# Kernel tuning notes

Measured on AMD Instinct MI355X. Metric: run time of the kernel, lower is better.

## Reference

```python
import jax, jax.numpy as jnp
import numpy as np

CLASS_COUNT = 21
THRESHOLD = 0.5
ALPHA = 0.25
GAMMA = 2.0
VARIANCE = (0.1, 0.2)

B, A, N_OBJ = 32, 24576, 16


def point_form(boxes):
    # center form (cx, cy, w, h) -> point form (xmin, ymin, xmax, ymax)
    return jnp.concatenate([boxes[:, :2] - boxes[:, 2:] / 2,
                            boxes[:, :2] + boxes[:, 2:] / 2], axis=1)


def jaccard(truths, priors):
    # truths [N,4], priors [A,4] both in point form -> IoU [N, A]
    lt = jnp.maximum(truths[:, None, :2], priors[None, :, :2])
    rb = jnp.minimum(truths[:, None, 2:], priors[None, :, 2:])
    wh = jnp.clip(rb - lt, 0.0, None)
    inter = wh[..., 0] * wh[..., 1]
    area_t = ((truths[:, 2] - truths[:, 0]) * (truths[:, 3] - truths[:, 1]))[:, None]
    area_p = ((priors[:, 2] - priors[:, 0]) * (priors[:, 3] - priors[:, 1]))[None, :]
    return inter / (area_t + area_p - inter)


def match_one(labels, truths, anchors):
    # labels [N] int, truths [N,4] point form, anchors [A,4] center form
    overlaps = jaccard(truths, point_form(anchors))           # [N, A]
    best_prior_idx = jnp.argmax(overlaps, axis=1)             # [N]
    best_truth_overlap = jnp.max(overlaps, axis=0)            # [A]
    best_truth_idx = jnp.argmax(overlaps, axis=0)             # [A]
    # ensure every gt matches its best prior
    best_truth_overlap = best_truth_overlap.at[best_prior_idx].set(2.0)
    best_truth_idx = best_truth_idx.at[best_prior_idx].set(jnp.arange(truths.shape[0]))
    matches = truths[best_truth_idx]                          # [A, 4]
    conf = jnp.where(best_truth_overlap < THRESHOLD, 0, labels[best_truth_idx])
    # encode with variances
    g_cxcy = ((matches[:, :2] + matches[:, 2:]) * 0.5 - anchors[:, :2]) / (VARIANCE[0] * anchors[:, 2:])
    g_wh = jnp.log((matches[:, 2:] - matches[:, :2]) / anchors[:, 2:]) / VARIANCE[1]
    return conf, jnp.concatenate([g_cxcy, g_wh], axis=1)


def setup_inputs() -> dict:
    key = jax.random.key(0)
    k1, k2, k3, k4, k5, k6, k7 = jax.random.split(key, 7)
    class_preds = jax.random.normal(k1, (B, A, CLASS_COUNT), dtype=jnp.float32)
    loc_preds = jax.random.normal(k2, (B, A, 4), dtype=jnp.float32)
    # ground-truth boxes: random valid point-form boxes in [0,1]
    ctr = jax.random.uniform(k3, (B, N_OBJ, 2), minval=0.2, maxval=0.8)
    wh = jax.random.uniform(k4, (B, N_OBJ, 2), minval=0.05, maxval=0.3)
    loc_targets = jnp.clip(jnp.concatenate([ctr - wh / 2, ctr + wh / 2], axis=-1), 0.0, 1.0)
    class_targets = jax.random.randint(k5, (B, N_OBJ), 1, CLASS_COUNT)
    # anchors in center form
    a_ctr = jax.random.uniform(k6, (A, 2), minval=0.05, maxval=0.95)
    a_wh = jax.random.uniform(k7, (A, 2), minval=0.05, maxval=0.4)
    anchors = jnp.concatenate([a_ctr, a_wh], axis=1)
    return {"class_preds": class_preds, "loc_preds": loc_preds,
            "loc_targets": loc_targets, "anchors": anchors,
            "class_targets": class_targets}


def reference(class_preds, loc_preds, loc_targets, anchors, class_targets):
    conf, loc_t = jax.vmap(match_one, in_axes=(0, 0, None))(class_targets, loc_targets, anchors)
    pos = conf > 0                                            # [B, A]
    num_matched = jnp.sum(pos).astype(jnp.float32)
    # smooth L1 over positive anchors (sum reduction, beta=1)
    d = loc_preds - loc_t
    ad = jnp.abs(d)
    sl1 = jnp.where(ad < 1.0, 0.5 * d * d, ad - 0.5)
    loc_loss = jnp.sum(sl1 * pos[..., None].astype(sl1.dtype))
    # focal loss (drop background column 0)
    cp = class_preds.reshape(-1, CLASS_COUNT)[:, 1:]          # [B*A, C-1]
    t = jax.nn.one_hot(conf.reshape(-1), CLASS_COUNT, dtype=cp.dtype)[:, 1:]
    p = jax.nn.sigmoid(cp)
    pt = jnp.where(t > 0, p, 1.0 - p)
    w = (1.0 - pt) ** GAMMA
    w = jnp.where(t > 0, ALPHA * w, (1.0 - ALPHA) * w)
    # stable binary cross entropy with logits, weighted, sum reduction
    bce = jnp.maximum(cp, 0.0) - cp * t + jnp.log1p(jnp.exp(-jnp.abs(cp)))
    class_loss = jnp.sum(w * bce)
    class_loss = class_loss / num_matched
    loc_loss = loc_loss / num_matched
    return jnp.stack([class_loss, loc_loss, class_loss + loc_loss])
```

## Files before the change

kernel.cpp:

```cpp
#include <hip/hip_runtime.h>

#define A_COUNT 24576
#define B_COUNT 32
#define NOBJ 16
#define C_COUNT 21

#define NCH 96
#define CHUNK (A_COUNT / NCH)
#define NBLK (NCH * B_COUNT)
#define TOTAL4 (B_COUNT * A_COUNT * C_COUNT / 4)
#define STRIDE4 (NBLK * 256)

#define WS_BPP 0
#define WS_LOCP 393216
#define WS_CLSP 405504
#define WS_POSP 417792
#define WS_DLOC 430080
#define WS_DCLS 430208
#define WS_DPOS 430336

__device__ __forceinline__ unsigned long long pack_key(float iou, int a) {
    unsigned int ib = __float_as_uint(iou);
    return ((unsigned long long)ib << 32) | (unsigned long long)(0xFFFFFFFFu - (unsigned int)a);
}

__device__ __forceinline__ float iou_pf(float tx0, float ty0, float tx1, float ty1, float at,
                                        float x0, float y0, float x1, float y1, float ap) {
    float lx = fmaxf(tx0, x0), ly = fmaxf(ty0, y0);
    float rx = fminf(tx1, x1), ry = fminf(ty1, y1);
    float w = fmaxf(rx - lx, 0.0f), h = fmaxf(ry - ly, 0.0f);
    float inter = w * h;
    return inter * __builtin_amdgcn_rcpf(at + ap - inter);
}

__device__ __forceinline__ float sl1(float d) {
    float ad = fabsf(d);
    return (ad < 1.0f) ? 0.5f * d * d : ad - 0.5f;
}

__device__ __forceinline__ float loc_term(float4 t, float4 an, float4 lp) {
    float gx = ((t.x + t.z) * 0.5f - an.x) / (0.1f * an.z);
    float gy = ((t.y + t.w) * 0.5f - an.y) / (0.1f * an.w);
    float gw = __logf((t.z - t.x) / an.z) * 5.0f;
    float gh = __logf((t.w - t.y) / an.w) * 5.0f;
    return sl1(lp.x - gx) + sl1(lp.y - gy) + sl1(lp.z - gw) + sl1(lp.w - gh);
}

__device__ __forceinline__ float corr_term(float x) {
    float E = __expf(x);
    float den = 1.0f + E;
    float s = __builtin_amdgcn_rcpf(den);
    float p = E * s;
    float L = __logf(den);
    return 0.25f * s * s * (L - x) - 0.75f * p * p * L;
}

#define FOC(xval, rr, acc) {                                 \
    float E_ = __expf(xval);                                 \
    float den_ = 1.0f + E_;                                  \
    float s_ = __builtin_amdgcn_rcpf(den_);                  \
    float p_ = E_ * s_;                                      \
    float L_ = __logf(den_);                                 \
    float v_ = ((rr) == 0 || (rr) == 21) ? 0.0f : p_ * p_ * L_; \
    acc += v_; }

__global__ __launch_bounds__(256, 8) void k_main(const float* __restrict__ cls,
                                                 const float4* __restrict__ locp,
                                                 const float4* __restrict__ anchors,
                                                 const float4* __restrict__ truths,
                                                 const int* __restrict__ labels,
                                                 unsigned long long* __restrict__ bp_partial,
                                                 float* __restrict__ loc_partial,
                                                 float* __restrict__ cls_partial,
                                                 unsigned int* __restrict__ pos_partial) {
    const int ch = blockIdx.x;
    const int b = blockIdx.y;
    const int tid = threadIdx.x;
    const int wv = tid >> 6, ln = tid & 63;
    __shared__ float4 s_t[NOBJ];
    __shared__ float s_area[NOBJ];
    __shared__ int s_lab[NOBJ];
    __shared__ unsigned long long s_w[NOBJ][4];
    if (tid < NOBJ) {
        float4 t = truths[b * NOBJ + tid];
        s_t[tid] = t;
        s_area[tid] = (t.z - t.x) * (t.w - t.y);
        s_lab[tid] = labels[b * NOBJ + tid];
    }
    __syncthreads();
    const int a0 = ch * CHUNK + tid;
    float4 an0 = anchors[a0];
    float p0x0 = an0.x - an0.z * 0.5f, p0y0 = an0.y - an0.w * 0.5f;
    float p0x1 = an0.x + an0.z * 0.5f, p0y1 = an0.y + an0.w * 0.5f;
    float ap0 = (p0x1 - p0x0) * (p0y1 - p0y0);
    float best0 = -1.0f;
    int idx0 = 0;
#pragma unroll
    for (int n = 0; n < NOBJ; ++n) {
        float4 t = s_t[n];
        float iou = iou_pf(t.x, t.y, t.z, t.w, s_area[n], p0x0, p0y0, p0x1, p0y1, ap0);
        if (iou > best0) { best0 = iou; idx0 = n; }
        float m = iou;
#pragma unroll
        for (int s = 32; s >= 1; s >>= 1) m = fmaxf(m, __shfl_xor(m, s));
        unsigned long long mask = __ballot(iou == m);
        if (ln == __builtin_ctzll(mask))
            s_w[n][wv] = pack_key(iou, a0);
    }
    __syncthreads();
    if (tid < NOBJ) {
        unsigned long long k = s_w[tid][0];
#pragma unroll
        for (int i = 1; i < 4; ++i) k = (s_w[tid][i] > k) ? s_w[tid][i] : k;
        bp_partial[(b * NOBJ + tid) * NCH + ch] = k;
    }
    float loc_l = 0.0f, corr_acc = 0.0f;
    unsigned int pos = 0;
    if (!(best0 < 0.5f)) {
        pos = 1;
        loc_l = loc_term(s_t[idx0], an0, locp[(size_t)b * A_COUNT + a0]);
        corr_acc = corr_term(cls[((size_t)b * A_COUNT + a0) * C_COUNT + s_lab[idx0]]);
    }

    const int bid = b * NCH + ch;
    float cls_acc;
    {
        const float4* cls4 = (const float4*)cls;
        int i = bid * 256 + tid;
        unsigned int f = (unsigned int)i * 4u;
        unsigned int dq = f / 21u;
        int r = (int)(f - dq * 21u);
        float acc0 = 0.0f, acc1 = 0.0f, acc2 = 0.0f, acc3 = 0.0f;
        for (; i < TOTAL4; i += STRIDE4) {
            float4 x4 = cls4[i];
            FOC(x4.x, r + 0, acc0); FOC(x4.y, r + 1, acc1);
            FOC(x4.z, r + 2, acc2); FOC(x4.w, r + 3, acc3);
            r += 12; if (r >= 21) r -= 21;
        }
        cls_acc = corr_acc + 0.75f * ((acc0 + acc1) + (acc2 + acc3));
    }

#pragma unroll
    for (int s = 32; s >= 1; s >>= 1) {
        loc_l += __shfl_xor(loc_l, s);
        cls_acc += __shfl_xor(cls_acc, s);
        pos += __shfl_xor(pos, s);
    }
    __shared__ float s_ll[4], s_cl[4];
    __shared__ unsigned int s_pp[4];
    if (ln == 0) {
        s_ll[wv] = loc_l;
        s_cl[wv] = cls_acc;
        s_pp[wv] = pos;
    }
    __syncthreads();
    if (tid == 0) {
        loc_partial[bid] = s_ll[0] + s_ll[1] + s_ll[2] + s_ll[3];
        cls_partial[bid] = s_cl[0] + s_cl[1] + s_cl[2] + s_cl[3];
        pos_partial[bid] = s_pp[0] + s_pp[1] + s_pp[2] + s_pp[3];
    }
}

__global__ __launch_bounds__(256) void k_fix(const float* __restrict__ cls,
                                             const float4* __restrict__ locp,
                                             const float4* __restrict__ anchors,
                                             const float4* __restrict__ truths,
                                             const int* __restrict__ labels,
                                             const unsigned long long* __restrict__ bp_partial,
                                             float* __restrict__ dloc,
                                             float* __restrict__ dcls,
                                             int* __restrict__ dpos) {
    const int b = blockIdx.x;
    const int tid = threadIdx.x;
    __shared__ int s_bp[NOBJ];
    {
        const int g = tid >> 4, l = tid & 15;
        const unsigned long long* pp = &bp_partial[(size_t)(b * NOBJ + g) * NCH];
        unsigned long long k = pp[l];
#pragma unroll
        for (int kk = 1; kk < 6; ++kk) {
            unsigned long long v = pp[l + 16 * kk];
            k = (v > k) ? v : k;
        }
#pragma unroll
        for (int s = 8; s >= 1; s >>= 1) {
            unsigned long long o = __shfl_xor(k, s);
            k = (o > k) ? o : k;
        }
        if (l == 0) {
            unsigned int ia = 0xFFFFFFFFu - (unsigned int)(k & 0xFFFFFFFFull);
            s_bp[g] = (ia >= A_COUNT) ? -1 : (int)ia;
        }
    }
    __syncthreads();
    float d_loc = 0.0f, d_cls = 0.0f;
    int d_pos = 0;
    if (tid < NOBJ) {
        const int n = tid;
        const int q = s_bp[n];
        bool winner = (q >= 0);
        for (int n2 = n + 1; n2 < NOBJ; ++n2)
            if (s_bp[n2] == q) winner = false;
        if (winner) {
            float4 an = anchors[q];
            float px0 = an.x - an.z * 0.5f, py0 = an.y - an.w * 0.5f;
            float px1 = an.x + an.z * 0.5f, py1 = an.y + an.w * 0.5f;
            float ap = (px1 - px0) * (py1 - py0);
            float best = -1.0f;
            int idx = 0;
            for (int n2 = 0; n2 < NOBJ; ++n2) {
                float4 t = truths[b * NOBJ + n2];
                float at = (t.z - t.x) * (t.w - t.y);
                float iou = iou_pf(t.x, t.y, t.z, t.w, at, px0, py0, px1, py1, ap);
                if (iou > best) { best = iou; idx = n2; }
            }
            float4 lp = locp[(size_t)b * A_COUNT + q];
            if (!(best < 0.5f)) {
                d_pos -= 1;
                d_loc -= loc_term(truths[b * NOBJ + idx], an, lp);
                d_cls -= corr_term(cls[((size_t)b * A_COUNT + q) * C_COUNT + labels[b * NOBJ + idx]]);
            }
            d_pos += 1;
            d_loc += loc_term(truths[b * NOBJ + n], an, lp);
            d_cls += corr_term(cls[((size_t)b * A_COUNT + q) * C_COUNT + labels[b * NOBJ + n]]);
        }
    }
    if (tid < 64) {
#pragma unroll
        for (int s = 8; s >= 1; s >>= 1) {
            d_loc += __shfl_xor(d_loc, s);
            d_cls += __shfl_xor(d_cls, s);
            d_pos += __shfl_xor(d_pos, s);
        }
        if (tid == 0) {
            dloc[b] = d_loc;
            dcls[b] = d_cls;
            dpos[b] = d_pos;
        }
    }
}

__global__ __launch_bounds__(256) void k_final(const float* __restrict__ loc_partial,
                                               const float* __restrict__ cls_partial,
                                               const unsigned int* __restrict__ pos_partial,
                                               const float* __restrict__ dloc,
                                               const float* __restrict__ dcls,
                                               const int* __restrict__ dpos,
                                               float* __restrict__ out) {
    const int tid = threadIdx.x;
    double loc = 0.0, clsv = 0.0;
    int pos = 0;
    for (int i = tid; i < NBLK; i += 256) {
        loc += (double)loc_partial[i];
        clsv += (double)cls_partial[i];
        pos += (int)pos_partial[i];
    }
    if (tid < B_COUNT) {
        loc += (double)dloc[tid];
        clsv += (double)dcls[tid];
        pos += dpos[tid];
    }
#pragma unroll
    for (int s = 32; s >= 1; s >>= 1) {
        loc += __shfl_xor(loc, s);
        clsv += __shfl_xor(clsv, s);
        pos += __shfl_xor(pos, s);
    }
    __shared__ double s_l[4], s_c[4];
    __shared__ int s_p[4];
    if ((tid & 63) == 0) {
        s_l[tid >> 6] = loc;
        s_c[tid >> 6] = clsv;
        s_p[tid >> 6] = pos;
    }
    __syncthreads();
    if (tid == 0) {
        double L = s_l[0] + s_l[1] + s_l[2] + s_l[3];
        double Cv = s_c[0] + s_c[1] + s_c[2] + s_c[3];
        float nm = (float)(s_p[0] + s_p[1] + s_p[2] + s_p[3]);
        float cf = (float)Cv / nm;
        float lf = (float)L / nm;
        out[0] = cf;
        out[1] = lf;
        out[2] = cf + lf;
    }
}

extern "C" void kernel_launch(void* const* d_in, const int* in_sizes, int n_in,
                              void* d_out, int out_size, void* d_ws, size_t ws_size,
                              hipStream_t stream) {
    const float* cls = (const float*)d_in[0];
    const float4* locp = (const float4*)d_in[1];
    const float4* truths = (const float4*)d_in[2];
    const float4* anchors = (const float4*)d_in[3];
    const int* labels = (const int*)d_in[4];

    char* ws = (char*)d_ws;
    unsigned long long* bp_partial = (unsigned long long*)(ws + WS_BPP);
    float* loc_partial = (float*)(ws + WS_LOCP);
    float* cls_partial = (float*)(ws + WS_CLSP);
    unsigned int* pos_partial = (unsigned int*)(ws + WS_POSP);
    float* dloc = (float*)(ws + WS_DLOC);
    float* dcls = (float*)(ws + WS_DCLS);
    int* dpos = (int*)(ws + WS_DPOS);

    k_main<<<dim3(NCH, B_COUNT), 256, 0, stream>>>(cls, locp, anchors, truths, labels,
                                                   bp_partial, loc_partial, cls_partial, pos_partial);
    k_fix<<<B_COUNT, 256, 0, stream>>>(cls, locp, anchors, truths, labels, bp_partial,
                                       dloc, dcls, dpos);
    k_final<<<1, 256, 0, stream>>>(loc_partial, cls_partial, pos_partial, dloc, dcls, dpos,
                                   (float*)d_out);
}
```

Before: 48.85 us.

## Split focal-loss streaming and anchor matching into separate block roles

The fused kernel now launches two kinds of blocks in one grid. 2048 blocks stream the class logits and accumulate the dense focal term, while 1536 matching blocks each handle two anchors per thread and emit the positive-anchor corrections, loc loss and counts. Separating the roles keeps the IoU/ballot matching work off the bandwidth-bound streaming blocks, and halving the matching block count shrinks the best-prior partials k_fix must reduce. The risk is that the two block types finish unevenly, and per-thread register pressure rises in the matching path.

New measurement: 46.15 us. -5.5%, faster.

```diff
diff --git a/kernel.cpp b/kernel.cpp
--- a/kernel.cpp
+++ b/kernel.cpp
@@ -5,19 +5,22 @@
 #define NOBJ 16
 #define C_COUNT 21
 
-#define NCH 96
-#define CHUNK (A_COUNT / NCH)
-#define NBLK (NCH * B_COUNT)
+#define NM 48
+#define CHUNK (A_COUNT / NM)
+#define NBLK_M (NM * B_COUNT)
+#define NBLK_F 2048
+#define GRID (NBLK_F + NBLK_M)
 #define TOTAL4 (B_COUNT * A_COUNT * C_COUNT / 4)
-#define STRIDE4 (NBLK * 256)
+#define STRIDE4F (NBLK_F * 256)
 
 #define WS_BPP 0
-#define WS_LOCP 393216
-#define WS_CLSP 405504
-#define WS_POSP 417792
-#define WS_DLOC 430080
-#define WS_DCLS 430208
-#define WS_DPOS 430336
+#define WS_LOCP 196608
+#define WS_CORP 202752
+#define WS_POSP 208896
+#define WS_CLSP 215040
+#define WS_DLOC 223232
+#define WS_DCLS 223360
+#define WS_DPOS 223488
 
 __device__ __forceinline__ unsigned long long pack_key(float iou, int a) {
     unsigned int ib = __float_as_uint(iou);
@@ -64,19 +67,46 @@
     float v_ = ((rr) == 0 || (rr) == 21) ? 0.0f : p_ * p_ * L_; \
     acc += v_; }
 
-__global__ __launch_bounds__(256, 8) void k_main(const float* __restrict__ cls,
-                                                 const float4* __restrict__ locp,
-                                                 const float4* __restrict__ anchors,
-                                                 const float4* __restrict__ truths,
-                                                 const int* __restrict__ labels,
-                                                 unsigned long long* __restrict__ bp_partial,
-                                                 float* __restrict__ loc_partial,
-                                                 float* __restrict__ cls_partial,
-                                                 unsigned int* __restrict__ pos_partial) {
-    const int ch = blockIdx.x;
-    const int b = blockIdx.y;
+__global__ __launch_bounds__(256, 8) void k_phase1(const float* __restrict__ cls,
+                                                   const float4* __restrict__ locp,
+                                                   const float4* __restrict__ anchors,
+                                                   const float4* __restrict__ truths,
+                                                   const int* __restrict__ labels,
+                                                   unsigned long long* __restrict__ bp_partial,
+                                                   float* __restrict__ loc_partial,
+                                                   float* __restrict__ corr_partial,
+                                                   unsigned int* __restrict__ pos_partial,
+                                                   float* __restrict__ cls_partial) {
+    const int bid = blockIdx.x;
     const int tid = threadIdx.x;
     const int wv = tid >> 6, ln = tid & 63;
+    __shared__ float s_red[4];
+
+    if (bid < NBLK_F) {
+        const float4* cls4 = (const float4*)cls;
+        float acc0 = 0.0f, acc1 = 0.0f, acc2 = 0.0f, acc3 = 0.0f;
+        int i = bid * 256 + tid;
+        unsigned int f = (unsigned int)i * 4u;
+        unsigned int dq = f / 21u;
+        int r = (int)(f - dq * 21u);
+        for (; i < TOTAL4; i += STRIDE4F) {
+            float4 x4 = cls4[i];
+            FOC(x4.x, r + 0, acc0); FOC(x4.y, r + 1, acc1);
+            FOC(x4.z, r + 2, acc2); FOC(x4.w, r + 3, acc3);
+            r += 8; if (r >= 21) r -= 21;
+        }
+        float cls_acc = 0.75f * ((acc0 + acc1) + (acc2 + acc3));
+#pragma unroll
+        for (int s = 32; s >= 1; s >>= 1) cls_acc += __shfl_xor(cls_acc, s);
+        if (ln == 0) s_red[wv] = cls_acc;
+        __syncthreads();
+        if (tid == 0) cls_partial[bid] = s_red[0] + s_red[1] + s_red[2] + s_red[3];
+        return;
+    }
+
+    const int mb = bid - NBLK_F;
+    const int ch = mb % NM;
+    const int b = mb / NM;
     __shared__ float4 s_t[NOBJ];
     __shared__ float s_area[NOBJ];
     __shared__ int s_lab[NOBJ];
@@ -89,75 +119,71 @@
     }
     __syncthreads();
     const int a0 = ch * CHUNK + tid;
+    const int a1 = a0 + 256;
     float4 an0 = anchors[a0];
+    float4 an1 = anchors[a1];
     float p0x0 = an0.x - an0.z * 0.5f, p0y0 = an0.y - an0.w * 0.5f;
     float p0x1 = an0.x + an0.z * 0.5f, p0y1 = an0.y + an0.w * 0.5f;
     float ap0 = (p0x1 - p0x0) * (p0y1 - p0y0);
-    float best0 = -1.0f;
-    int idx0 = 0;
+    float p1x0 = an1.x - an1.z * 0.5f, p1y0 = an1.y - an1.w * 0.5f;
+    float p1x1 = an1.x + an1.z * 0.5f, p1y1 = an1.y + an1.w * 0.5f;
+    float ap1 = (p1x1 - p1x0) * (p1y1 - p1y0);
+    float best0 = -1.0f, best1 = -1.0f;
+    int idx0 = 0, idx1 = 0;
 #pragma unroll
     for (int n = 0; n < NOBJ; ++n) {
         float4 t = s_t[n];
-        float iou = iou_pf(t.x, t.y, t.z, t.w, s_area[n], p0x0, p0y0, p0x1, p0y1, ap0);
-        if (iou > best0) { best0 = iou; idx0 = n; }
-        float m = iou;
+        float at = s_area[n];
+        float iou0 = iou_pf(t.x, t.y, t.z, t.w, at, p0x0, p0y0, p0x1, p0y1, ap0);
+        float iou1 = iou_pf(t.x, t.y, t.z, t.w, at, p1x0, p1y0, p1x1, p1y1, ap1);
+        if (iou0 > best0) { best0 = iou0; idx0 = n; }
+        if (iou1 > best1) { best1 = iou1; idx1 = n; }
+        float lm = fmaxf(iou0, iou1);
+        float m = lm;
 #pragma unroll
         for (int s = 32; s >= 1; s >>= 1) m = fmaxf(m, __shfl_xor(m, s));
-        unsigned long long mask = __ballot(iou == m);
-        if (ln == __builtin_ctzll(mask))
-            s_w[n][wv] = pack_key(iou, a0);
+        unsigned long long mask = __ballot(lm == m);
+        if (ln == __builtin_ctzll(mask)) {
+            s_w[n][wv] = (iou0 == m) ? pack_key(iou0, a0) : pack_key(iou1, a1);
+        }
     }
     __syncthreads();
     if (tid < NOBJ) {
         unsigned long long k = s_w[tid][0];
 #pragma unroll
         for (int i = 1; i < 4; ++i) k = (s_w[tid][i] > k) ? s_w[tid][i] : k;
-        bp_partial[(b * NOBJ + tid) * NCH + ch] = k;
+        bp_partial[(b * NOBJ + tid) * NM + ch] = k;
     }
     float loc_l = 0.0f, corr_acc = 0.0f;
     unsigned int pos = 0;
     if (!(best0 < 0.5f)) {
-        pos = 1;
-        loc_l = loc_term(s_t[idx0], an0, locp[(size_t)b * A_COUNT + a0]);
-        corr_acc = corr_term(cls[((size_t)b * A_COUNT + a0) * C_COUNT + s_lab[idx0]]);
-    }
-
-    const int bid = b * NCH + ch;
-    float cls_acc;
-    {
-        const float4* cls4 = (const float4*)cls;
-        int i = bid * 256 + tid;
-        unsigned int f = (unsigned int)i * 4u;
-        unsigned int dq = f / 21u;
-        int r = (int)(f - dq * 21u);
-        float acc0 = 0.0f, acc1 = 0.0f, acc2 = 0.0f, acc3 = 0.0f;
-        for (; i < TOTAL4; i += STRIDE4) {
-            float4 x4 = cls4[i];
-            FOC(x4.x, r + 0, acc0); FOC(x4.y, r + 1, acc1);
-            FOC(x4.z, r + 2, acc2); FOC(x4.w, r + 3, acc3);
-            r += 12; if (r >= 21) r -= 21;
-        }
-        cls_acc = corr_acc + 0.75f * ((acc0 + acc1) + (acc2 + acc3));
-    }
-
+        pos++;
+        loc_l += loc_term(s_t[idx0], an0, locp[(size_t)b * A_COUNT + a0]);
+        corr_acc += corr_term(cls[((size_t)b * A_COUNT + a0) * C_COUNT + s_lab[idx0]]);
+    }
+    if (!(best1 < 0.5f)) {
+        pos++;
+        loc_l += loc_term(s_t[idx1], an1, locp[(size_t)b * A_COUNT + a1]);
+        corr_acc += corr_term(cls[((size_t)b * A_COUNT + a1) * C_COUNT + s_lab[idx1]]);
+    }
 #pragma unroll
     for (int s = 32; s >= 1; s >>= 1) {
         loc_l += __shfl_xor(loc_l, s);
-        cls_acc += __shfl_xor(cls_acc, s);
+        corr_acc += __shfl_xor(corr_acc, s);
         pos += __shfl_xor(pos, s);
     }
-    __shared__ float s_ll[4], s_cl[4];
+    __shared__ float s_cr[4];
     __shared__ unsigned int s_pp[4];
     if (ln == 0) {
-        s_ll[wv] = loc_l;
-        s_cl[wv] = cls_acc;
+        s_red[wv] = loc_l;
+        s_cr[wv] = corr_acc;
         s_pp[wv] = pos;
     }
     __syncthreads();
     if (tid == 0) {
-        loc_partial[bid] = s_ll[0] + s_ll[1] + s_ll[2] + s_ll[3];
-        cls_partial[bid] = s_cl[0] + s_cl[1] + s_cl[2] + s_cl[3];
-        pos_partial[bid] = s_pp[0] + s_pp[1] + s_pp[2] + s_pp[3];
+        loc_partial[mb] = s_red[0] + s_red[1] + s_red[2] + s_red[3];
+        corr_partial[mb] = s_cr[0] + s_cr[1] + s_cr[2] + s_cr[3];
+        pos_partial[mb] = s_pp[0] + s_pp[1] + s_pp[2] + s_pp[3];
     }
 }
 
@@ -175,10 +201,10 @@
     __shared__ int s_bp[NOBJ];
     {
         const int g = tid >> 4, l = tid & 15;
-        const unsigned long long* pp = &bp_partial[(size_t)(b * NOBJ + g) * NCH];
+        const unsigned long long* pp = &bp_partial[(size_t)(b * NOBJ + g) * NM];
         unsigned long long k = pp[l];
 #pragma unroll
-        for (int kk = 1; kk < 6; ++kk) {
+        for (int kk = 1; kk < 3; ++kk) {
             unsigned long long v = pp[l + 16 * kk];
             k = (v > k) ? v : k;
         }
@@ -241,8 +267,9 @@
 }
 
 __global__ __launch_bounds__(256) void k_final(const float* __restrict__ loc_partial,
+                                               const float* __restrict__ corr_partial,
+                                               const unsigned int* __restrict__ pos_partial,
                                                const float* __restrict__ cls_partial,
-                                               const unsigned int* __restrict__ pos_partial,
                                                const float* __restrict__ dloc,
                                                const float* __restrict__ dcls,
                                                const int* __restrict__ dpos,
@@ -250,11 +277,12 @@
     const int tid = threadIdx.x;
     double loc = 0.0, clsv = 0.0;
     int pos = 0;
-    for (int i = tid; i < NBLK; i += 256) {
+    for (int i = tid; i < NBLK_M; i += 256) {
         loc += (double)loc_partial[i];
-        clsv += (double)cls_partial[i];
+        clsv += (double)corr_partial[i];
         pos += (int)pos_partial[i];
     }
+    for (int i = tid; i < NBLK_F; i += 256) clsv += (double)cls_partial[i];
     if (tid < B_COUNT) {
         loc += (double)dloc[tid];
         clsv += (double)dcls[tid];
@@ -298,16 +326,17 @@
     char* ws = (char*)d_ws;
     unsigned long long* bp_partial = (unsigned long long*)(ws + WS_BPP);
     float* loc_partial = (float*)(ws + WS_LOCP);
+    float* corr_partial = (float*)(ws + WS_CORP);
+    unsigned int* pos_partial = (unsigned int*)(ws + WS_POSP);
     float* cls_partial = (float*)(ws + WS_CLSP);
-    unsigned int* pos_partial = (unsigned int*)(ws + WS_POSP);
     float* dloc = (float*)(ws + WS_DLOC);
     float* dcls = (float*)(ws + WS_DCLS);
     int* dpos = (int*)(ws + WS_DPOS);
 
-    k_main<<<dim3(NCH, B_COUNT), 256, 0, stream>>>(cls, locp, anchors, truths, labels,
-                                                   bp_partial, loc_partial, cls_partial, pos_partial);
+    k_phase1<<<GRID, 256, 0, stream>>>(cls, locp, anchors, truths, labels, bp_partial,
+                                       loc_partial, corr_partial, pos_partial, cls_partial);
     k_fix<<<B_COUNT, 256, 0, stream>>>(cls, locp, anchors, truths, labels, bp_partial,
                                        dloc, dcls, dpos);
-    k_final<<<1, 256, 0, stream>>>(loc_partial, cls_partial, pos_partial, dloc, dcls, dpos,
-                                   (float*)d_out);
-}
+    k_final<<<1, 256, 0, stream>>>(loc_partial, corr_partial, pos_partial, cls_partial,
+                                   dloc, dcls, dpos, (float*)d_out);
+}
```
